# Optimization experiments

Hardware: AMD Instinct MI355X
Metric: run time of the kernel (lower is better)

Reference implementation:

```python
import jax, jax.numpy as jnp
import numpy as np

B, N_INST, H, W = 8, 64, 480, 480
EPS = 1e-12  # torch F.normalize eps


def setup_inputs() -> dict:
    key = jax.random.key(0)
    k1, k2, k3, k4, k5, k6 = jax.random.split(key, 6)
    # binary instance masks (output of connected-component labeling in the original)
    instance_masks = (jax.random.uniform(k1, (N_INST, H, W)) < 0.3).astype(jnp.float32)
    sample_ids = jax.random.randint(k2, (N_INST,), 0, B, dtype=jnp.int64)
    quaternion = jax.random.normal(k3, (B, 4, H, W), dtype=jnp.float32)
    scales = jax.random.normal(k4, (B, 3, H, W), dtype=jnp.float32)
    xy = jax.random.normal(k5, (B, 2, H, W), dtype=jnp.float32)
    z = jax.random.normal(k6, (B, H, W), dtype=jnp.float32)
    return {"instance_masks": instance_masks, "sample_ids": sample_ids,
            "quaternion": quaternion, "scales": scales, "xy": xy, "z": z}


def reference(instance_masks, sample_ids, quaternion, scales, xy, z):
    # instance_masks: [N,H,W] binary float; sample_ids: [N] in [0,B)
    mask_size = jnp.sum(instance_masks, axis=(-2, -1))  # [N]

    def masked_mean(d):  # d: [N,C,H,W] -> [N,C]
        return jnp.einsum('nhw,nchw->nc', instance_masks, d) / mask_size[:, None]

    # quaternion: masked mean then L2-normalize along channel dim
    q_agg = masked_mean(quaternion[sample_ids])                       # [N,4]
    q_agg = q_agg / jnp.maximum(jnp.linalg.norm(q_agg, axis=1, keepdims=True), EPS)
    # scales: masked mean
    s_agg = masked_mean(scales[sample_ids])                           # [N,3]
    # z: masked mean of [N,1,H,W] then exp
    z_agg = jnp.exp(masked_mean(z[sample_ids][:, None]))              # [N,1]
    # xy: masked dense map (passed on to hough voting downstream)
    xy_masked = instance_masks[:, None] * xy[sample_ids]              # [N,2,H,W]
    return q_agg, s_agg, z_agg, xy_masked
```

## Files before the change

kernel.cpp:

```cpp
#include <hip/hip_runtime.h>
#include <math.h>

#define HW      (480 * 480)
#define HW4     (HW / 4)
#define NINST   64
#define NB      8
#define NV      9
#define GI      4
#define NBLK    128
#define THREADS 256

__device__ __forceinline__ float dot4(const float4 a, const float4 b) {
    return (a.x * b.x + a.y * b.y) + (a.z * b.z + a.w * b.w);
}

__global__ __launch_bounds__(THREADS) void agg_main(
    const float* __restrict__ masks,
    const int*   __restrict__ sids,
    const float* __restrict__ quat,
    const float* __restrict__ scales,
    const float* __restrict__ xy,
    const float* __restrict__ z,
    float*       __restrict__ out,
    float*       __restrict__ part)
{
    const int tid = threadIdx.x;
    const int bx  = blockIdx.x;
    const int b   = blockIdx.y;

    __shared__ int   ilist[NINST];
    __shared__ int   scnt;
    __shared__ float sred[4][GI * NV];

    if (tid == 0) {
        int c = 0;
        for (int n = 0; n < NINST; ++n)
            if (sids[n] == b) ilist[c++] = n;
        scnt = c;
    }
    __syncthreads();
    const int cnt = scnt;

    const float4* M  = (const float4*)masks;
    const float4* Q  = (const float4*)quat   + (size_t)b * 4 * HW4;
    const float4* S  = (const float4*)scales + (size_t)b * 3 * HW4;
    const float4* X  = (const float4*)xy     + (size_t)b * 2 * HW4;
    const float4* Zp = (const float4*)z      + (size_t)b * HW4;
    float4*       O  = (float4*)(out + 512);

    const int lane = tid & 63;
    const int wid  = tid >> 6;

    for (int g0 = 0; g0 < cnt; g0 += GI) {
        int  nidx[GI];
        bool valid[GI];
#pragma unroll
        for (int j = 0; j < GI; ++j) {
            valid[j] = (g0 + j < cnt);
            nidx[j]  = ilist[valid[j] ? (g0 + j) : (cnt - 1)];
        }

        float acc[GI][NV];
#pragma unroll
        for (int j = 0; j < GI; ++j)
#pragma unroll
            for (int v = 0; v < NV; ++v) acc[j][v] = 0.0f;

        for (int i = bx * THREADS + tid; i < HW4; i += NBLK * THREADS) {
            float4 m[GI];
#pragma unroll
            for (int j = 0; j < GI; ++j)
                m[j] = M[(size_t)nidx[j] * HW4 + i];

            const float4 vx0 = X[i];
            const float4 vx1 = X[HW4 + i];
#pragma unroll
            for (int j = 0; j < GI; ++j) {
                if (valid[j]) {
                    O[((size_t)nidx[j] * 2 + 0) * HW4 + i] = make_float4(
                        m[j].x * vx0.x, m[j].y * vx0.y, m[j].z * vx0.z, m[j].w * vx0.w);
                    O[((size_t)nidx[j] * 2 + 1) * HW4 + i] = make_float4(
                        m[j].x * vx1.x, m[j].y * vx1.y, m[j].z * vx1.z, m[j].w * vx1.w);
                }
            }

#pragma unroll
            for (int j = 0; j < GI; ++j)
                acc[j][0] += (m[j].x + m[j].y) + (m[j].z + m[j].w);

            float4 t;
            t = Q[0 * HW4 + i];
#pragma unroll
            for (int j = 0; j < GI; ++j) acc[j][1] += dot4(m[j], t);
            t = Q[1 * HW4 + i];
#pragma unroll
            for (int j = 0; j < GI; ++j) acc[j][2] += dot4(m[j], t);
            t = Q[2 * HW4 + i];
#pragma unroll
            for (int j = 0; j < GI; ++j) acc[j][3] += dot4(m[j], t);
            t = Q[3 * HW4 + i];
#pragma unroll
            for (int j = 0; j < GI; ++j) acc[j][4] += dot4(m[j], t);
            t = S[0 * HW4 + i];
#pragma unroll
            for (int j = 0; j < GI; ++j) acc[j][5] += dot4(m[j], t);
            t = S[1 * HW4 + i];
#pragma unroll
            for (int j = 0; j < GI; ++j) acc[j][6] += dot4(m[j], t);
            t = S[2 * HW4 + i];
#pragma unroll
            for (int j = 0; j < GI; ++j) acc[j][7] += dot4(m[j], t);
            t = Zp[i];
#pragma unroll
            for (int j = 0; j < GI; ++j) acc[j][8] += dot4(m[j], t);
        }

#pragma unroll
        for (int j = 0; j < GI; ++j)
#pragma unroll
            for (int v = 0; v < NV; ++v) {
                float x = acc[j][v];
#pragma unroll
                for (int off = 32; off > 0; off >>= 1)
                    x += __shfl_down(x, off, 64);
                if (lane == 0) sred[wid][j * NV + v] = x;
            }
        __syncthreads();
        if (tid < GI * NV) {
            const int j = tid / NV;
            const int v = tid - j * NV;
            if (g0 + j < cnt) {
                const int n = ilist[g0 + j];
                part[((size_t)n * NBLK + bx) * NV + v] =
                    (sred[0][tid] + sred[1][tid]) + (sred[2][tid] + sred[3][tid]);
            }
        }
        __syncthreads();
    }
}

__global__ __launch_bounds__(THREADS) void agg_final(
    const float* __restrict__ part,
    float*       __restrict__ out)
{
    const int n   = blockIdx.x;
    const int tid = threadIdx.x;

    float vals[NV];
#pragma unroll
    for (int v = 0; v < NV; ++v) vals[v] = 0.0f;
    for (int c = tid; c < NBLK; c += THREADS) {
        const float* p = part + ((size_t)n * NBLK + c) * NV;
#pragma unroll
        for (int v = 0; v < NV; ++v) vals[v] += p[v];
    }

    __shared__ float sred[4][NV];
    const int lane = tid & 63;
    const int wid  = tid >> 6;
#pragma unroll
    for (int v = 0; v < NV; ++v) {
        float x = vals[v];
#pragma unroll
        for (int off = 32; off > 0; off >>= 1)
            x += __shfl_down(x, off, 64);
        if (lane == 0) sred[wid][v] = x;
    }
    __syncthreads();

    if (tid == 0) {
        float s[NV];
#pragma unroll
        for (int v = 0; v < NV; ++v)
            s[v] = (sred[0][v] + sred[1][v]) + (sred[2][v] + sred[3][v]);

        const float inv = 1.0f / s[0];
        const float q0 = s[1] * inv, q1 = s[2] * inv, q2 = s[3] * inv, q3 = s[4] * inv;
        const float norm = sqrtf(q0 * q0 + q1 * q1 + q2 * q2 + q3 * q3);
        const float d = fmaxf(norm, 1e-12f);
        out[n * 4 + 0] = q0 / d;
        out[n * 4 + 1] = q1 / d;
        out[n * 4 + 2] = q2 / d;
        out[n * 4 + 3] = q3 / d;

        out[256 + n * 3 + 0] = s[5] * inv;
        out[256 + n * 3 + 1] = s[6] * inv;
        out[256 + n * 3 + 2] = s[7] * inv;

        out[448 + n] = expf(s[8] * inv);
    }
}

extern "C" void kernel_launch(void* const* d_in, const int* in_sizes, int n_in,
                              void* d_out, int out_size, void* d_ws, size_t ws_size,
                              hipStream_t stream) {
    const float* masks  = (const float*)d_in[0];
    const int*   sids   = (const int*)d_in[1];
    const float* quat   = (const float*)d_in[2];
    const float* scales = (const float*)d_in[3];
    const float* xy     = (const float*)d_in[4];
    const float* z      = (const float*)d_in[5];
    float* out  = (float*)d_out;
    float* part = (float*)d_ws;

    dim3 grid(NBLK, NB);
    agg_main<<<grid, THREADS, 0, stream>>>(masks, sids, quat, scales, xy, z, out, part);
    agg_final<<<NINST, THREADS, 0, stream>>>(part, out);
}
```

Before: 262.0 us.

## Load per-pixel data once per thread and use DPP wave reductions

Sets the grid to 225 blocks so each thread covers exactly one float4 of the image. The quaternion, scale, xy and z values are then loaded into registers once and reused across every instance group, instead of being reloaded inside a strided loop for each group. The instance group size grows from 4 to 8, and the shuffle-based wave reduction is replaced with DPP row operations that read the total from lane 63. This cuts redundant feature reads at the cost of higher register pressure, and it adds more partial sums for the final kernel to combine.

```diff
diff --git a/kernel.cpp b/kernel.cpp
--- a/kernel.cpp
+++ b/kernel.cpp
@@ -6,12 +6,27 @@
 #define NINST   64
 #define NB      8
 #define NV      9
-#define GI      4
-#define NBLK    128
+#define GI      8
+#define NBLK    225
 #define THREADS 256
 
 __device__ __forceinline__ float dot4(const float4 a, const float4 b) {
     return (a.x * b.x + a.y * b.y) + (a.z * b.z + a.w * b.w);
+}
+
+template <int CTRL>
+__device__ __forceinline__ float dpp_add(float x) {
+    int s = __builtin_amdgcn_update_dpp(0, __float_as_int(x), CTRL, 0xf, 0xf, false);
+    return x + __int_as_float(s);
+}
+__device__ __forceinline__ float wave_sum(float x) {
+    x = dpp_add<0x111>(x);
+    x = dpp_add<0x112>(x);
+    x = dpp_add<0x114>(x);
+    x = dpp_add<0x118>(x);
+    x = dpp_add<0x142>(x);
+    x = dpp_add<0x143>(x);
+    return x;
 }
 
 __global__ __launch_bounds__(THREADS) void agg_main(
@@ -27,10 +42,11 @@
     const int tid = threadIdx.x;
     const int bx  = blockIdx.x;
     const int b   = blockIdx.y;
+    const int i   = bx * THREADS + tid;
 
     __shared__ int   ilist[NINST];
     __shared__ int   scnt;
-    __shared__ float sred[4][GI * NV];
+    __shared__ float swred[4][GI * NV];
 
     if (tid == 0) {
         int c = 0;
@@ -48,6 +64,17 @@
     const float4* Zp = (const float4*)z      + (size_t)b * HW4;
     float4*       O  = (float4*)(out + 512);
 
+    const float4 vq0 = Q[0 * HW4 + i];
+    const float4 vq1 = Q[1 * HW4 + i];
+    const float4 vq2 = Q[2 * HW4 + i];
+    const float4 vq3 = Q[3 * HW4 + i];
+    const float4 vs0 = S[0 * HW4 + i];
+    const float4 vs1 = S[1 * HW4 + i];
+    const float4 vs2 = S[2 * HW4 + i];
+    const float4 vx0 = X[0 * HW4 + i];
+    const float4 vx1 = X[1 * HW4 + i];
+    const float4 vz  = Zp[i];
+
     const int lane = tid & 63;
     const int wid  = tid >> 6;
 
@@ -60,70 +87,41 @@
             nidx[j]  = ilist[valid[j] ? (g0 + j) : (cnt - 1)];
         }
 
+        float4 m[GI];
+#pragma unroll
+        for (int j = 0; j < GI; ++j)
+            m[j] = M[(size_t)nidx[j] * HW4 + i];
+
+#pragma unroll
+        for (int j = 0; j < GI; ++j) {
+            if (valid[j]) {
+                O[((size_t)nidx[j] * 2 + 0) * HW4 + i] = make_float4(
+                    m[j].x * vx0.x, m[j].y * vx0.y, m[j].z * vx0.z, m[j].w * vx0.w);
+                O[((size_t)nidx[j] * 2 + 1) * HW4 + i] = make_float4(
+                    m[j].x * vx1.x, m[j].y * vx1.y, m[j].z * vx1.z, m[j].w * vx1.w);
+            }
+        }
+
         float acc[GI][NV];
 #pragma unroll
+        for (int j = 0; j < GI; ++j) {
+            acc[j][0] = (m[j].x + m[j].y) + (m[j].z + m[j].w);
+            acc[j][1] = dot4(m[j], vq0);
+            acc[j][2] = dot4(m[j], vq1);
+            acc[j][3] = dot4(m[j], vq2);
+            acc[j][4] = dot4(m[j], vq3);
+            acc[j][5] = dot4(m[j], vs0);
+            acc[j][6] = dot4(m[j], vs1);
+            acc[j][7] = dot4(m[j], vs2);
+            acc[j][8] = dot4(m[j], vz);
+        }
+
+#pragma unroll
         for (int j = 0; j < GI; ++j)
 #pragma unroll
-            for (int v = 0; v < NV; ++v) acc[j][v] = 0.0f;
-
-        for (int i = bx * THREADS + tid; i < HW4; i += NBLK * THREADS) {
-            float4 m[GI];
-#pragma unroll
-            for (int j = 0; j < GI; ++j)
-                m[j] = M[(size_t)nidx[j] * HW4 + i];
-
-            const float4 vx0 = X[i];
-            const float4 vx1 = X[HW4 + i];
-#pragma unroll
-            for (int j = 0; j < GI; ++j) {
-                if (valid[j]) {
-                    O[((size_t)nidx[j] * 2 + 0) * HW4 + i] = make_float4(
-                        m[j].x * vx0.x, m[j].y * vx0.y, m[j].z * vx0.z, m[j].w * vx0.w);
-                    O[((size_t)nidx[j] * 2 + 1) * HW4 + i] = make_float4(
-                        m[j].x * vx1.x, m[j].y * vx1.y, m[j].z * vx1.z, m[j].w * vx1.w);
-                }
-            }
-
-#pragma unroll
-            for (int j = 0; j < GI; ++j)
-                acc[j][0] += (m[j].x + m[j].y) + (m[j].z + m[j].w);
-
-            float4 t;
-            t = Q[0 * HW4 + i];
-#pragma unroll
-            for (int j = 0; j < GI; ++j) acc[j][1] += dot4(m[j], t);
-            t = Q[1 * HW4 + i];
-#pragma unroll
-            for (int j = 0; j < GI; ++j) acc[j][2] += dot4(m[j], t);
-            t = Q[2 * HW4 + i];
-#pragma unroll
-            for (int j = 0; j < GI; ++j) acc[j][3] += dot4(m[j], t);
-            t = Q[3 * HW4 + i];
-#pragma unroll
-            for (int j = 0; j < GI; ++j) acc[j][4] += dot4(m[j], t);
-            t = S[0 * HW4 + i];
-#pragma unroll
-            for (int j = 0; j < GI; ++j) acc[j][5] += dot4(m[j], t);
-            t = S[1 * HW4 + i];
-#pragma unroll
-            for (int j = 0; j < GI; ++j) acc[j][6] += dot4(m[j], t);
-            t = S[2 * HW4 + i];
-#pragma unroll
-            for (int j = 0; j < GI; ++j) acc[j][7] += dot4(m[j], t);
-            t = Zp[i];
-#pragma unroll
-            for (int j = 0; j < GI; ++j) acc[j][8] += dot4(m[j], t);
-        }
-
-#pragma unroll
-        for (int j = 0; j < GI; ++j)
-#pragma unroll
             for (int v = 0; v < NV; ++v) {
-                float x = acc[j][v];
-#pragma unroll
-                for (int off = 32; off > 0; off >>= 1)
-                    x += __shfl_down(x, off, 64);
-                if (lane == 0) sred[wid][j * NV + v] = x;
+                const float t = wave_sum(acc[j][v]);
+                if (lane == 63) swred[wid][j * NV + v] = t;
             }
         __syncthreads();
         if (tid < GI * NV) {
@@ -132,7 +130,7 @@
             if (g0 + j < cnt) {
                 const int n = ilist[g0 + j];
                 part[((size_t)n * NBLK + bx) * NV + v] =
-                    (sred[0][tid] + sred[1][tid]) + (sred[2][tid] + sred[3][tid]);
+                    (swred[0][tid] + swred[1][tid]) + (swred[2][tid] + swred[3][tid]);
             }
         }
         __syncthreads();
```

New measurement: 245.7 us. 1.07x faster.
